# Performance work log

Hardware: AMD Instinct MI355X
Metric: run time of the kernel (lower is better)

The kernel has to match this reference:

```python
import jax, jax.numpy as jnp
import numpy as np

EPS = 1e-5

def _conv(x, w, pad, groups=1):
    return jax.lax.conv_general_dilated(
        x, w, window_strides=(1, 1), padding=[(pad, pad), (pad, pad)],
        dimension_numbers=('NCHW', 'OIHW', 'NCHW'), feature_group_count=groups)

def _bn(x, g, b, m, v):
    # inference batch-norm, per-channel
    s = g * jax.lax.rsqrt(v + EPS)
    return x * s[None, :, None, None] + (b - m * s)[None, :, None, None]

def setup_inputs() -> dict:
    key = jax.random.key(0)
    ks = jax.random.split(key, 20)
    B, C, H, W = 32, 128, 64, 64
    cs = C // 2  # c_split = 64
    d = {
        'x': jax.random.normal(ks[0], (B, C, H, W), jnp.float32),
        'weights': jax.random.uniform(ks[1], (B, 2), jnp.float32),
        'indices': jax.random.randint(ks[2], (B, 2), 0, 4, jnp.int32),
        # expert 0: Conv(cs -> C, k=3, p=1) + BN + SiLU
        'e0_w': jax.random.normal(ks[3], (C, cs, 3, 3), jnp.float32) * 0.05,
        'e0_g': jax.random.uniform(ks[4], (C,), jnp.float32, 0.5, 1.5),
        'e0_b': jax.random.normal(ks[5], (C,), jnp.float32) * 0.1,
        'e0_m': jax.random.normal(ks[6], (C,), jnp.float32) * 0.1,
        'e0_v': jax.random.uniform(ks[7], (C,), jnp.float32, 0.5, 1.5),
        # expert 1: depthwise 5x5 (cs, groups=cs) -> 1x1 (cs -> C) -> BN -> SiLU
        'e1_dw': jax.random.normal(ks[8], (cs, 1, 5, 5), jnp.float32) * 0.05,
        'e1_pw': jax.random.normal(ks[9], (C, cs, 1, 1), jnp.float32) * 0.05,
        'e1_g': jax.random.uniform(ks[10], (C,), jnp.float32, 0.5, 1.5),
        'e1_b': jax.random.normal(ks[11], (C,), jnp.float32) * 0.1,
        'e1_m': jax.random.normal(ks[12], (C,), jnp.float32) * 0.1,
        'e1_v': jax.random.uniform(ks[13], (C,), jnp.float32, 0.5, 1.5),
        # expert 2: GhostConv(C -> C): cv1 = Conv(C, C//2, 3), cv2 = Conv(C//2, C//2, 5, groups=C//2)
        'e2a_w': jax.random.normal(ks[14], (cs, C, 3, 3), jnp.float32) * 0.05,
        'e2a_g': jax.random.uniform(ks[15], (cs,), jnp.float32, 0.5, 1.5),
        'e2a_b': jax.random.normal(ks[16], (cs,), jnp.float32) * 0.1,
        'e2a_m': jax.random.normal(ks[17], (cs,), jnp.float32) * 0.1,
        'e2a_v': jax.random.uniform(ks[18], (cs,), jnp.float32, 0.5, 1.5),
        'e2b_w': jax.random.normal(ks[19], (cs, 1, 5, 5), jnp.float32) * 0.05,
    }
    ks2 = jax.random.split(jax.random.key(1), 4)
    d['e2b_g'] = jax.random.uniform(ks2[0], (cs,), jnp.float32, 0.5, 1.5)
    d['e2b_b'] = jax.random.normal(ks2[1], (cs,), jnp.float32) * 0.1
    d['e2b_m'] = jax.random.normal(ks2[2], (cs,), jnp.float32) * 0.1
    d['e2b_v'] = jax.random.uniform(ks2[3], (cs,), jnp.float32, 0.5, 1.5)
    return d

def _forward(x, weights, indices,
             e0_w, e0_g, e0_b, e0_m, e0_v,
             e1_dw, e1_pw, e1_g, e1_b, e1_m, e1_v,
             e2a_w, e2a_g, e2a_b, e2a_m, e2a_v,
             e2b_w, e2b_g, e2b_b, e2b_m, e2b_v):
    C = x.shape[1]
    cs = C // 2
    x_rgb, x_ir = x[:, :cs], x[:, cs:]
    # expert outputs computed densely over the whole batch, masked combine below
    e0 = jax.nn.silu(_bn(_conv(x_rgb, e0_w, pad=1), e0_g, e0_b, e0_m, e0_v))
    e1 = jax.nn.silu(_bn(_conv(_conv(x_ir, e1_dw, pad=2, groups=cs), e1_pw, pad=0),
                         e1_g, e1_b, e1_m, e1_v))
    g1 = jax.nn.silu(_bn(_conv(x, e2a_w, pad=1), e2a_g, e2a_b, e2a_m, e2a_v))
    g2 = jax.nn.silu(_bn(_conv(g1, e2b_w, pad=2, groups=cs), e2b_g, e2b_b, e2b_m, e2b_v))
    e2 = jnp.concatenate([g1, g2], axis=1)
    out = jnp.zeros_like(x)
    K = indices.shape[1]
    for k in range(K):  # small fixed top-k loop
        idx = indices[:, k][:, None, None, None]          # [B,1,1,1]
        w = weights[:, k][:, None, None, None]            # [B,1,1,1]
        out = out + jnp.where(idx == 0, e0 * w, 0.0)
        out = out + jnp.where(idx == 1, e1 * w, 0.0)
        out = out + jnp.where(idx == 2, e2 * w, 0.0)
        out = out + jnp.where(idx == 3, x * 0.1, 0.0)
    return out

def reference(x, weights, indices,
              e0_w, e0_g, e0_b, e0_m, e0_v,
              e1_dw, e1_pw, e1_g, e1_b, e1_m, e1_v,
              e2a_w, e2a_g, e2a_b, e2a_m, e2a_v,
              e2b_w, e2b_g, e2b_b, e2b_m, e2b_v):
    return _forward(x, weights, indices,
                    e0_w, e0_g, e0_b, e0_m, e0_v,
                    e1_dw, e1_pw, e1_g, e1_b, e1_m, e1_v,
                    e2a_w, e2a_g, e2a_b, e2a_m, e2a_v,
                    e2b_w, e2b_g, e2b_b, e2b_m, e2b_v)
```

## Files before the change

kernel.cpp:

```cpp
#include <hip/hip_runtime.h>

#define B_  32
#define C_  128
#define CS  64
#define H_  64
#define W_  64
#define HW  (H_*W_)

typedef __attribute__((ext_vector_type(8))) short bf16x8_t;
typedef __attribute__((ext_vector_type(4))) float f32x4_t;
typedef unsigned short u16;
typedef unsigned int   u32;

__device__ __forceinline__ float silu_f(float v) { return v / (1.f + __expf(-v)); }

__device__ __forceinline__ u16 f2bf(float f) {
    u32 u = __float_as_uint(f);
    u = (u + 0x7FFFu + ((u >> 16) & 1u)) >> 16;
    return (u16)u;
}
__device__ __forceinline__ float bf2f(u16 u) {
    return __uint_as_float(((u32)u) << 16);
}
__device__ __forceinline__ u32 cvtpk(float a, float b) {
    u32 r;
    asm("v_cvt_pk_bf16_f32 %0, %1, %2" : "=v"(r) : "v"(a), "v"(b));
    return r;
}

__device__ __forceinline__ void get_coeffs(const float* __restrict__ wts,
                                           const int* __restrict__ idxs, int b,
                                           float& c0, float& c1, float& c2, float& cid) {
    int   i0 = idxs[b*2+0], i1 = idxs[b*2+1];
    float w0 = wts[b*2+0],  w1 = wts[b*2+1];
    c0  = (i0==0?w0:0.f)   + (i1==0?w1:0.f);
    c1  = (i0==1?w0:0.f)   + (i1==1?w1:0.f);
    c2  = (i0==2?w0:0.f)   + (i1==2?w1:0.f);
    cid = (i0==3?0.1f:0.f) + (i1==3?0.1f:0.f);
}

__global__ __launch_bounds__(256) void k_prep(
    const float* __restrict__ e0w, const float* __restrict__ e2aw, const float* __restrict__ e1pw,
    u16* __restrict__ Wt0f, u16* __restrict__ Wt2f, u16* __restrict__ Wt1f)
{
    const int i0 = blockIdx.x*256 + threadIdx.x, stride = gridDim.x*256;
    for (int i = i0; i < 73728; i += stride) {
        int j = i&7, lane = (i>>3)&63, cog = (i>>9)&7, kc = (i>>12)&1, tap = i>>13;
        int co = cog*16 + (lane&15), ci = kc*32 + (lane>>4)*8 + j;
        Wt0f[i] = f2bf(e0w[(size_t)(co*64 + ci)*9 + tap]);
    }
    for (int i = i0; i < 73728; i += stride) {
        int j = i&7, lane = (i>>3)&63, cog = (i>>9)&3, kc = (i>>11)&3, tap = i>>13;
        int co = cog*16 + (lane&15), ci = kc*32 + (lane>>4)*8 + j;
        Wt2f[i] = f2bf(e2aw[(size_t)(co*128 + ci)*9 + tap]);
    }
    for (int i = i0; i < 8192; i += stride) {
        int j = i&7, lane = (i>>3)&63, cog = (i>>9)&7, kc = (i>>12)&1;
        int co = cog*16 + (lane&15), ci = kc*32 + (lane>>4)*8 + j;
        Wt1f[i] = f2bf(e1pw[(size_t)co*64 + ci]);
    }
}

__device__ __forceinline__ void stage_x(
    const float* __restrict__ xb,
    char* lin, int orow0, int t)
{
    f32x4_t V0[8], V1[8];
    #pragma unroll
    for (int k = 0; k < 8; ++k) {
        const int u = t + k*256;
        const int quad = u & 15, r = (u >> 4) & 3, cp = u >> 6;
        const int hh = orow0 - 1 + r;
        const int hcl = (hh < 0) ? 0 : ((hh > 63) ? 63 : hh);
        const float* p0 = xb + (size_t)(2*cp)*HW + hcl*64 + quad*4;
        asm volatile("global_load_dwordx4 %0, %1, off" : "=v"(V0[k]) : "v"(p0));
        asm volatile("global_load_dwordx4 %0, %1, off" : "=v"(V1[k]) : "v"(p0 + HW));
    }
    asm volatile("s_waitcnt vmcnt(0)" ::: "memory");
    __builtin_amdgcn_sched_barrier(0);
    #pragma unroll
    for (int k = 0; k < 8; ++k) {
        const int u = t + k*256;
        const int quad = u & 15, r = (u >> 4) & 3, cp = u >> 6;
        const int hh = orow0 - 1 + r;
        const bool ok = (hh >= 0 && hh < H_);
        #pragma unroll
        for (int j = 0; j < 4; ++j) {
            const int p = r*66 + quad*4 + j + 1;
            const u32 a = ((u32)p*128 + (u32)cp*4) ^ (((u32)(p & 7)) << 4);
            float f0 = ok ? V0[k][j] : 0.f;
            float f1 = ok ? V1[k][j] : 0.f;
            *(u32*)(lin + a) = cvtpk(f0, f1);
        }
    }
    {
        const int cp = t & 31, side = (t >> 5) & 1, r = t >> 6;
        const int p = r*66 + side*65;
        const u32 a = ((u32)p*128 + (u32)cp*4) ^ (((u32)(p & 7)) << 4);
        *(u32*)(lin + a) = 0u;
    }
}

template<int NCF, int NPF, int TK, int COUT>
__device__ __forceinline__ void conv_pass(
    const char* lin, const u16* __restrict__ wb, int koff,
    int rbase, int pxbase, int l15, int kg,
    f32x4_t (&acc)[NCF][NPF])
{
    bf16x8_t A0[NCF], A1[NCF], A2[NCF];

    auto issueA = [&](int i, bf16x8_t (&dst)[NCF]) {
        const int tap = i >> 1, kcl = i & 1;
        const u16* wt = wb + (size_t)((tap*TK + koff + kcl)*(COUT/16))*512;
        #pragma unroll
        for (int cf = 0; cf < NCF; ++cf)
            asm volatile("global_load_dwordx4 %0, %1, off"
                         : "=v"(dst[cf]) : "v"(wt + ((size_t)cf << 9)));
    };
    auto ldsB = [&](int i, int pf) -> bf16x8_t {
        const int tap = i >> 1, kcl = i & 1;
        const int dh = tap / 3, dwp = tap % 3;
        const int p = (rbase + dh)*66 + pxbase + pf*16 + l15 + dwp;
        u32 a = (u32)p*128 + (u32)kcl*64 + (u32)kg*16;
        a ^= ((u32)(p & 7)) << 4;
        return *(const bf16x8_t*)(lin + a);
    };

    issueA(0, A0);
    issueA(1, A1);
    #pragma unroll
    for (int i = 0; i < 18; ++i) {
        if (i + 2 < 18) {
            const int s = (i + 2) % 3;
            if (s == 0)      issueA(i + 2, A0);
            else if (s == 1) issueA(i + 2, A1);
            else             issueA(i + 2, A2);
        }
        if (i < 16)       asm volatile("s_waitcnt vmcnt(8)" ::: "memory");
        else if (i == 16) asm volatile("s_waitcnt vmcnt(4)" ::: "memory");
        else              asm volatile("s_waitcnt vmcnt(0)" ::: "memory");
        __builtin_amdgcn_sched_barrier(0);
        bf16x8_t* ac = (i % 3 == 0) ? A0 : ((i % 3 == 1) ? A1 : A2);
        #pragma unroll
        for (int pf = 0; pf < NPF; ++pf) {
            bf16x8_t bfr = ldsB(i, pf);
            #pragma unroll
            for (int cf = 0; cf < NCF; ++cf)
                acc[cf][pf] = __builtin_amdgcn_mfma_f32_16x16x32_bf16(ac[cf], bfr, acc[cf][pf], 0, 0, 0);
        }
    }
}

__global__ __launch_bounds__(256, 3) void k_conv(
    const float* __restrict__ x,
    const float* __restrict__ wts, const int* __restrict__ idxs,
    const u16* __restrict__ Wt0f, const u16* __restrict__ Wt2f,
    const float* __restrict__ e0g, const float* __restrict__ e0b,
    const float* __restrict__ e0m, const float* __restrict__ e0v,
    const float* __restrict__ e2ag, const float* __restrict__ e2ab,
    const float* __restrict__ e2am, const float* __restrict__ e2av,
    float* __restrict__ out, u16* __restrict__ g1)
{
    __shared__ char lin[33792];
    const int b = blockIdx.y, orow0 = blockIdx.x*2, t = threadIdx.x;
    float c0, c1, c2, cid;
    get_coeffs(wts, idxs, b, c0, c1, c2, cid);

    const int lane = t & 63, l15 = lane & 15, kg = lane >> 4, wv = t >> 6;
    const float* xb = x + (size_t)b*C_*HW;

    if (blockIdx.z == 0) {
        if (c0 == 0.f) {
            for (int i = t; i < 4096; i += 256) {
                int ch = i >> 5, q = i & 31;
                size_t o = ((size_t)(b*C_+ch))*HW + (size_t)orow0*64 + q*4;
                float4 ov;
                if (cid != 0.f) {
                    float4 xv = *(const float4*)(x + o);
                    ov.x = cid*xv.x; ov.y = cid*xv.y; ov.z = cid*xv.z; ov.w = cid*xv.w;
                } else { ov.x = ov.y = ov.z = ov.w = 0.f; }
                *(float4*)(out + o) = ov;
            }
            return;
        }
        stage_x(xb, lin, orow0, t);
        __syncthreads();

        const int cw = wv >> 1, rw = wv & 1;
        const int cobase = cw*64;
        f32x4_t acc[4][4];
        #pragma unroll
        for (int cf = 0; cf < 4; ++cf)
            #pragma unroll
            for (int pf = 0; pf < 4; ++pf)
                acc[cf][pf] = (f32x4_t){0.f, 0.f, 0.f, 0.f};

        const u16* wb = Wt0f + (size_t)(cobase >> 4)*512 + (size_t)lane*8;
        conv_pass<4, 4, 2, 128>(lin, wb, 0, rw, 0, l15, kg, acc);

        #pragma unroll
        for (int cf = 0; cf < 4; ++cf) {
            float sarr[4], tarr[4];
            #pragma unroll
            for (int r = 0; r < 4; ++r) {
                int co = cobase + cf*16 + kg*4 + r;
                float s = e0g[co] * rsqrtf(e0v[co] + 1e-5f);
                sarr[r] = s; tarr[r] = e0b[co] - e0m[co]*s;
            }
            #pragma unroll
            for (int pf = 0; pf < 4; ++pf) {
                size_t rowoff = (size_t)(orow0 + rw)*64 + pf*16 + l15;
                #pragma unroll
                for (int r = 0; r < 4; ++r) {
                    int co = cobase + cf*16 + kg*4 + r;
                    float v = silu_f(acc[cf][pf][r]*sarr[r] + tarr[r]);
                    size_t o = ((size_t)(b*C_+co))*HW + rowoff;
                    float idv = (cid != 0.f) ? cid*x[o] : 0.f;
                    out[o] = c0*v + idv;
                }
            }
        }
    } else {
        if (c2 == 0.f) return;

        const int rw = wv >> 1, pw = wv & 1;
        const int pxbase = pw*32;
        f32x4_t acc[4][2];
        #pragma unroll
        for (int cf = 0; cf < 4; ++cf)
            #pragma unroll
            for (int pf = 0; pf < 2; ++pf)
                acc[cf][pf] = (f32x4_t){0.f, 0.f, 0.f, 0.f};

        const u16* wb = Wt2f + (size_t)lane*8;

        stage_x(xb, lin, orow0, t);
        __syncthreads();
        conv_pass<4, 2, 4, 64>(lin, wb, 0, rw, pxbase, l15, kg, acc);
        __syncthreads();
        stage_x(xb + (size_t)CS*HW, lin, orow0, t);
        __syncthreads();
        conv_pass<4, 2, 4, 64>(lin, wb, 2, rw, pxbase, l15, kg, acc);

        #pragma unroll
        for (int cf = 0; cf < 4; ++cf) {
            float sarr[4], tarr[4];
            #pragma unroll
            for (int r = 0; r < 4; ++r) {
                int co = cf*16 + kg*4 + r;
                float s = e2ag[co] * rsqrtf(e2av[co] + 1e-5f);
                sarr[r] = s; tarr[r] = e2ab[co] - e2am[co]*s;
            }
            #pragma unroll
            for (int pf = 0; pf < 2; ++pf) {
                size_t rowoff = (size_t)(orow0 + rw)*64 + pxbase + pf*16 + l15;
                #pragma unroll
                for (int r = 0; r < 4; ++r) {
                    int co = cf*16 + kg*4 + r;
                    float v = silu_f(acc[cf][pf][r]*sarr[r] + tarr[r]);
                    g1[((size_t)(b*CS+co))*HW + rowoff] = f2bf(v);
                }
            }
        }
    }
}

__global__ __launch_bounds__(256) void k_tail(
    const float* __restrict__ x, const u16* __restrict__ g1,
    const float* __restrict__ wts, const int* __restrict__ idxs,
    const float* __restrict__ e1dw, const u16* __restrict__ Wt1f,
    const float* __restrict__ e1g, const float* __restrict__ e1b,
    const float* __restrict__ e1m, const float* __restrict__ e1v,
    const float* __restrict__ e2bw,
    const float* __restrict__ e2bg, const float* __restrict__ e2bb,
    const float* __restrict__ e2bm, const float* __restrict__ e2bv,
    float* __restrict__ out)
{
    const int b = blockIdx.y, band = blockIdx.x, t = threadIdx.x;
    const int orow0 = band*2;

    float c0, c1, c2, cid;
    get_coeffs(wts, idxs, b, c0, c1, c2, cid);
    if (c1 == 0.f && c2 == 0.f) return;

    __shared__ u16  lin[6*64*70];
    __shared__ u16  lout[128*72];
    __shared__ float wl[64*26];

    const int lane = t & 63, chl = lane & 15, cs = lane >> 4;
    const int wv = t >> 6, outrow = wv & 1, chhalf = wv >> 1;
    const int l15 = lane & 15, kg = lane >> 4;

    if (c1 != 0.f) {
        for (int i = t; i < 64*25; i += 256) wl[(i/25)*26 + (i%25)] = e1dw[i];
        for (int i = t; i < 6*64*16; i += 256) {
            int q = i & 15, ch = (i >> 4) & 63, r = i >> 10;
            int hh = orow0 - 2 + r;
            u32 w0 = 0u, w1 = 0u;
            if (hh >= 0 && hh < H_) {
                float4 v = *(const float4*)(x + ((size_t)(b*C_ + CS + ch))*HW + hh*64 + q*4);
                w0 = cvtpk(v.x, v.y); w1 = cvtpk(v.z, v.w);
            }
            u32* dst = (u32*)&lin[(r*64 + ch)*70 + 2 + q*4];
            dst[0] = w0; dst[1] = w1;
        }
        for (int i = t; i < 6*64; i += 256) {
            int ch = i & 63, r = i >> 6;
            *(u32*)&lin[(r*64 + ch)*70]      = 0u;
            u32* e = (u32*)&lin[(r*64 + ch)*70 + 66];
            e[0] = 0u; e[1] = 0u;
        }
        __syncthreads();

        #pragma unroll
        for (int chi = 0; chi < 2; ++chi) {
            const int ch = chhalf*32 + chl + chi*16;
            const float* wch = &wl[ch*26];
            float accp[16];
            #pragma unroll
            for (int p = 0; p < 16; ++p) accp[p] = 0.f;
            #pragma unroll
            for (int kh = 0; kh < 5; ++kh) {
                const u16* src = &lin[((outrow + kh)*64 + ch)*70 + cs*16];
                float rb[20];
                #pragma unroll
                for (int k = 0; k < 10; ++k) {
                    u32 u = *(const u32*)(src + 2*k);
                    rb[2*k]   = __uint_as_float(u << 16);
                    rb[2*k+1] = __uint_as_float(u & 0xFFFF0000u);
                }
                #pragma unroll
                for (int kw = 0; kw < 5; ++kw) {
                    float wvv = wch[kh*5 + kw];
                    #pragma unroll
                    for (int p = 0; p < 16; ++p) accp[p] += rb[p+kw]*wvv;
                }
            }
            const int px0 = outrow*64 + cs*16;
            #pragma unroll
            for (int p = 0; p < 16; ++p) lout[(px0+p)*72 + ch] = f2bf(accp[p]);
        }
        __syncthreads();

        const int cw = wv >> 1, pwv = wv & 1;
        f32x4_t acc[4][4];
        #pragma unroll
        for (int cf = 0; cf < 4; ++cf)
            #pragma unroll
            for (int pf = 0; pf < 4; ++pf)
                acc[cf][pf] = (f32x4_t){0.f, 0.f, 0.f, 0.f};

        #pragma unroll
        for (int kc = 0; kc < 2; ++kc) {
            const u16* wt = Wt1f + (((size_t)(kc*8 + cw*4)) << 9) + lane*8;
            bf16x8_t af[4];
            #pragma unroll
            for (int cf = 0; cf < 4; ++cf) af[cf] = *(const bf16x8_t*)(wt + (cf << 9));
            const int k0 = kc*32 + kg*8;
            #pragma unroll
            for (int pf = 0; pf < 4; ++pf) {
                bf16x8_t bfr = *(const bf16x8_t*)&lout[(pwv*64 + pf*16 + l15)*72 + k0];
                #pragma unroll
                for (int cf = 0; cf < 4; ++cf)
                    acc[cf][pf] = __builtin_amdgcn_mfma_f32_16x16x32_bf16(af[cf], bfr, acc[cf][pf], 0, 0, 0);
            }
        }

        #pragma unroll
        for (int cf = 0; cf < 4; ++cf) {
            float sarr[4], tarr[4];
            #pragma unroll
            for (int r = 0; r < 4; ++r) {
                int co = cw*64 + cf*16 + kg*4 + r;
                float s = e1g[co] * rsqrtf(e1v[co] + 1e-5f);
                sarr[r] = s; tarr[r] = e1b[co] - e1m[co]*s;
            }
            #pragma unroll
            for (int pf = 0; pf < 4; ++pf) {
                int px = pwv*64 + pf*16 + l15;
                size_t rowoff = (size_t)(orow0 + (px>>6))*64 + (px&63);
                #pragma unroll
                for (int r = 0; r < 4; ++r) {
                    int co = cw*64 + cf*16 + kg*4 + r;
                    float v = silu_f(acc[cf][pf][r]*sarr[r] + tarr[r]);
                    out[((size_t)(b*C_+co))*HW + rowoff] += c1*v;
                }
            }
        }
    }

    if (c2 != 0.f) {
        __syncthreads();

        for (int i = t; i < 64*25; i += 256) wl[(i/25)*26 + (i%25)] = e2bw[i];
        for (int i = t; i < 6*64*16; i += 256) {
            int q = i & 15, ch = (i >> 4) & 63, r = i >> 10;
            int hh = orow0 - 2 + r;
            u32 w0 = 0u, w1 = 0u;
            if (hh >= 0 && hh < H_) {
                const u32* src = (const u32*)(g1 + ((size_t)(b*CS+ch))*HW + hh*64 + q*4);
                w0 = src[0]; w1 = src[1];
            }
            u32* dst = (u32*)&lin[(r*64 + ch)*70 + 2 + q*4];
            dst[0] = w0; dst[1] = w1;
        }
        for (int i = t; i < 6*64; i += 256) {
            int ch = i & 63, r = i >> 6;
            *(u32*)&lin[(r*64 + ch)*70] = 0u;
            u32* e = (u32*)&lin[(r*64 + ch)*70 + 66];
            e[0] = 0u; e[1] = 0u;
        }
        __syncthreads();

        for (int i = t; i < 2*64*16; i += 256) {
            int q = i & 15, ch = (i >> 4) & 63, r = i >> 10;
            const u16* src = &lin[((r+2)*64 + ch)*70 + 2 + q*4];
            float* op = out + ((size_t)(b*C_+ch))*HW + (size_t)(orow0+r)*64 + q*4;
            float4 ov = *(float4*)op;
            ov.x += c2*bf2f(src[0]); ov.y += c2*bf2f(src[1]);
            ov.z += c2*bf2f(src[2]); ov.w += c2*bf2f(src[3]);
            *(float4*)op = ov;
        }

        #pragma unroll
        for (int chi = 0; chi < 2; ++chi) {
            const int ch = chhalf*32 + chl + chi*16;
            const float* wch = &wl[ch*26];
            float accp[16];
            #pragma unroll
            for (int p = 0; p < 16; ++p) accp[p] = 0.f;
            #pragma unroll
            for (int kh = 0; kh < 5; ++kh) {
                const u16* src = &lin[((outrow + kh)*64 + ch)*70 + cs*16];
                float rb[20];
                #pragma unroll
                for (int k = 0; k < 10; ++k) {
                    u32 u = *(const u32*)(src + 2*k);
                    rb[2*k]   = __uint_as_float(u << 16);
                    rb[2*k+1] = __uint_as_float(u & 0xFFFF0000u);
                }
                #pragma unroll
                for (int kw = 0; kw < 5; ++kw) {
                    float wvv = wch[kh*5 + kw];
                    #pragma unroll
                    for (int p = 0; p < 16; ++p) accp[p] += rb[p+kw]*wvv;
                }
            }
            float s = e2bg[ch] * rsqrtf(e2bv[ch] + 1e-5f);
            float tt = e2bb[ch] - e2bm[ch]*s;
            float* op = out + ((size_t)(b*C_ + CS + ch))*HW + (size_t)(orow0+outrow)*64 + cs*16;
            #pragma unroll
            for (int q = 0; q < 4; ++q) {
                float4 ov = *(float4*)(op + q*4);
                ov.x += c2*silu_f(accp[q*4+0]*s + tt);
                ov.y += c2*silu_f(accp[q*4+1]*s + tt);
                ov.z += c2*silu_f(accp[q*4+2]*s + tt);
                ov.w += c2*silu_f(accp[q*4+3]*s + tt);
                *(float4*)(op + q*4) = ov;
            }
        }
    }
}

extern "C" void kernel_launch(void* const* d_in, const int* in_sizes, int n_in,
                              void* d_out, int out_size, void* d_ws, size_t ws_size,
                              hipStream_t stream) {
    const float* x    = (const float*)d_in[0];
    const float* wts  = (const float*)d_in[1];
    const int*   idxs = (const int*)  d_in[2];
    const float* e0w  = (const float*)d_in[3];
    const float* e0g  = (const float*)d_in[4];
    const float* e0b  = (const float*)d_in[5];
    const float* e0m  = (const float*)d_in[6];
    const float* e0v  = (const float*)d_in[7];
    const float* e1dw = (const float*)d_in[8];
    const float* e1pw = (const float*)d_in[9];
    const float* e1g  = (const float*)d_in[10];
    const float* e1b  = (const float*)d_in[11];
    const float* e1m  = (const float*)d_in[12];
    const float* e1v  = (const float*)d_in[13];
    const float* e2aw = (const float*)d_in[14];
    const float* e2ag = (const float*)d_in[15];
    const float* e2ab = (const float*)d_in[16];
    const float* e2am = (const float*)d_in[17];
    const float* e2av = (const float*)d_in[18];
    const float* e2bw = (const float*)d_in[19];
    const float* e2bg = (const float*)d_in[20];
    const float* e2bb = (const float*)d_in[21];
    const float* e2bm = (const float*)d_in[22];
    const float* e2bv = (const float*)d_in[23];

    float* out = (float*)d_out;

    u16* g1   = (u16*)d_ws;
    u16* Wt0f = g1 + (size_t)8388608;
    u16* Wt2f = Wt0f + 73728;
    u16* Wt1f = Wt2f + 73728;

    k_prep<<<128, 256, 0, stream>>>(e0w, e2aw, e1pw, Wt0f, Wt2f, Wt1f);
    k_conv<<<dim3(32, B_, 2), 256, 0, stream>>>(
        x, wts, idxs, Wt0f, Wt2f,
        e0g, e0b, e0m, e0v, e2ag, e2ab, e2am, e2av, out, g1);
    k_tail<<<dim3(32, B_), 256, 0, stream>>>(
        x, g1, wts, idxs, e1dw, Wt1f, e1g, e1b, e1m, e1v,
        e2bw, e2bg, e2bb, e2bm, e2bv, out);
}
```

Before: 97.08 us.

## Compact active conv work into a worklist consumed by persistent atomic-fetching blocks

The prep kernel now builds a compacted list of active work items (expert-0 conv bands, GhostConv cv1 bands, identity/zero-fill bands) from the routing indices. k_conv becomes a persistent kernel of 1024 blocks that grab items through a global atomic counter, instead of launching a full 3D grid where inactive blocks exit early. Occupancy is raised via launch bounds 4 to fit more resident blocks. This is meant to remove wasted block launches and tail imbalance, at the cost of atomic contention, extra barriers per item and possible register pressure from the higher occupancy target.

```diff
diff --git a/kernel.cpp b/kernel.cpp
--- a/kernel.cpp
+++ b/kernel.cpp
@@ -41,7 +41,9 @@
 
 __global__ __launch_bounds__(256) void k_prep(
     const float* __restrict__ e0w, const float* __restrict__ e2aw, const float* __restrict__ e1pw,
-    u16* __restrict__ Wt0f, u16* __restrict__ Wt2f, u16* __restrict__ Wt1f)
+    const float* __restrict__ wts, const int* __restrict__ idxs,
+    u16* __restrict__ Wt0f, u16* __restrict__ Wt2f, u16* __restrict__ Wt1f,
+    u32* __restrict__ wl)
 {
     const int i0 = blockIdx.x*256 + threadIdx.x, stride = gridDim.x*256;
     for (int i = i0; i < 73728; i += stride) {
@@ -58,6 +60,33 @@
         int j = i&7, lane = (i>>3)&63, cog = (i>>9)&7, kc = (i>>12)&1;
         int co = cog*16 + (lane&15), ci = kc*32 + (lane>>4)*8 + j;
         Wt1f[i] = f2bf(e1pw[(size_t)co*64 + ci]);
+    }
+
+    if (blockIdx.x == 0) {
+        __shared__ u32 base[3][32];
+        if (threadIdx.x == 0) {
+            u32 n = 0;
+            for (int tp = 0; tp < 3; ++tp)
+                for (int bb = 0; bb < 32; ++bb) {
+                    float c0, c1, c2, cid;
+                    get_coeffs(wts, idxs, bb, c0, c1, c2, cid);
+                    bool act = (tp == 0) ? (c0 != 0.f) : (tp == 1) ? (c2 != 0.f) : (c0 == 0.f);
+                    base[tp][bb] = act ? n : 0xFFFFFFFFu;
+                    if (act) n += 32;
+                }
+            wl[0] = 0u;
+            wl[1] = n;
+        }
+        __syncthreads();
+        if (threadIdx.x < 32) {
+            for (int tp = 0; tp < 3; ++tp)
+                for (int bb = 0; bb < 32; ++bb) {
+                    u32 bs = base[tp][bb];
+                    if (bs != 0xFFFFFFFFu)
+                        wl[2 + bs + threadIdx.x] =
+                            ((u32)tp << 12) | ((u32)bb << 5) | (u32)threadIdx.x;
+                }
+        }
     }
 }
 
@@ -151,7 +180,7 @@
     }
 }
 
-__global__ __launch_bounds__(256, 3) void k_conv(
+__global__ __launch_bounds__(256, 4) void k_conv(
     const float* __restrict__ x,
     const float* __restrict__ wts, const int* __restrict__ idxs,
     const u16* __restrict__ Wt0f, const u16* __restrict__ Wt2f,
@@ -159,18 +188,28 @@
     const float* __restrict__ e0m, const float* __restrict__ e0v,
     const float* __restrict__ e2ag, const float* __restrict__ e2ab,
     const float* __restrict__ e2am, const float* __restrict__ e2av,
-    float* __restrict__ out, u16* __restrict__ g1)
+    float* __restrict__ out, u16* __restrict__ g1, u32* __restrict__ wl)
 {
     __shared__ char lin[33792];
-    const int b = blockIdx.y, orow0 = blockIdx.x*2, t = threadIdx.x;
-    float c0, c1, c2, cid;
-    get_coeffs(wts, idxs, b, c0, c1, c2, cid);
-
+    __shared__ u32 s_item;
+    const int t = threadIdx.x;
+    const u32 n_items = wl[1];
     const int lane = t & 63, l15 = lane & 15, kg = lane >> 4, wv = t >> 6;
-    const float* xb = x + (size_t)b*C_*HW;
-
-    if (blockIdx.z == 0) {
-        if (c0 == 0.f) {
+
+    for (;;) {
+        __syncthreads();
+        if (t == 0) s_item = atomicAdd(&wl[0], 1u);
+        __syncthreads();
+        const u32 ii = s_item;
+        if (ii >= n_items) return;
+        const u32 item = wl[2 + ii];
+        const int tp = item >> 12, b = (item >> 5) & 31, band = item & 31;
+        const int orow0 = band*2;
+        float c0, c1, c2, cid;
+        get_coeffs(wts, idxs, b, c0, c1, c2, cid);
+        const float* xb = x + (size_t)b*C_*HW;
+
+        if (tp == 2) {
             for (int i = t; i < 4096; i += 256) {
                 int ch = i >> 5, q = i & 31;
                 size_t o = ((size_t)(b*C_+ch))*HW + (size_t)orow0*64 + q*4;
@@ -181,84 +220,85 @@
                 } else { ov.x = ov.y = ov.z = ov.w = 0.f; }
                 *(float4*)(out + o) = ov;
             }
-            return;
-        }
-        stage_x(xb, lin, orow0, t);
-        __syncthreads();
-
-        const int cw = wv >> 1, rw = wv & 1;
-        const int cobase = cw*64;
-        f32x4_t acc[4][4];
-        #pragma unroll
-        for (int cf = 0; cf < 4; ++cf)
-            #pragma unroll
-            for (int pf = 0; pf < 4; ++pf)
-                acc[cf][pf] = (f32x4_t){0.f, 0.f, 0.f, 0.f};
-
-        const u16* wb = Wt0f + (size_t)(cobase >> 4)*512 + (size_t)lane*8;
-        conv_pass<4, 4, 2, 128>(lin, wb, 0, rw, 0, l15, kg, acc);
-
-        #pragma unroll
-        for (int cf = 0; cf < 4; ++cf) {
-            float sarr[4], tarr[4];
-            #pragma unroll
-            for (int r = 0; r < 4; ++r) {
-                int co = cobase + cf*16 + kg*4 + r;
-                float s = e0g[co] * rsqrtf(e0v[co] + 1e-5f);
-                sarr[r] = s; tarr[r] = e0b[co] - e0m[co]*s;
-            }
-            #pragma unroll
-            for (int pf = 0; pf < 4; ++pf) {
-                size_t rowoff = (size_t)(orow0 + rw)*64 + pf*16 + l15;
+            continue;
+        }
+
+        if (tp == 0) {
+            stage_x(xb, lin, orow0, t);
+            __syncthreads();
+
+            const int cw = wv >> 1, rw = wv & 1;
+            const int cobase = cw*64;
+            f32x4_t acc[4][4];
+            #pragma unroll
+            for (int cf = 0; cf < 4; ++cf)
+                #pragma unroll
+                for (int pf = 0; pf < 4; ++pf)
+                    acc[cf][pf] = (f32x4_t){0.f, 0.f, 0.f, 0.f};
+
+            const u16* wb = Wt0f + (size_t)(cobase >> 4)*512 + (size_t)lane*8;
+            conv_pass<4, 4, 2, 128>(lin, wb, 0, rw, 0, l15, kg, acc);
+
+            #pragma unroll
+            for (int cf = 0; cf < 4; ++cf) {
+                float sarr[4], tarr[4];
                 #pragma unroll
                 for (int r = 0; r < 4; ++r) {
                     int co = cobase + cf*16 + kg*4 + r;
-                    float v = silu_f(acc[cf][pf][r]*sarr[r] + tarr[r]);
-                    size_t o = ((size_t)(b*C_+co))*HW + rowoff;
-                    float idv = (cid != 0.f) ? cid*x[o] : 0.f;
-                    out[o] = c0*v + idv;
-                }
-            }
-        }
-    } else {
-        if (c2 == 0.f) return;
-
-        const int rw = wv >> 1, pw = wv & 1;
-        const int pxbase = pw*32;
-        f32x4_t acc[4][2];
-        #pragma unroll
-        for (int cf = 0; cf < 4; ++cf)
-            #pragma unroll
-            for (int pf = 0; pf < 2; ++pf)
-                acc[cf][pf] = (f32x4_t){0.f, 0.f, 0.f, 0.f};
-
-        const u16* wb = Wt2f + (size_t)lane*8;
-
-        stage_x(xb, lin, orow0, t);
-        __syncthreads();
-        conv_pass<4, 2, 4, 64>(lin, wb, 0, rw, pxbase, l15, kg, acc);
-        __syncthreads();
-        stage_x(xb + (size_t)CS*HW, lin, orow0, t);
-        __syncthreads();
-        conv_pass<4, 2, 4, 64>(lin, wb, 2, rw, pxbase, l15, kg, acc);
-
-        #pragma unroll
-        for (int cf = 0; cf < 4; ++cf) {
-            float sarr[4], tarr[4];
-            #pragma unroll
-            for (int r = 0; r < 4; ++r) {
-                int co = cf*16 + kg*4 + r;
-                float s = e2ag[co] * rsqrtf(e2av[co] + 1e-5f);
-                sarr[r] = s; tarr[r] = e2ab[co] - e2am[co]*s;
-            }
-            #pragma unroll
-            for (int pf = 0; pf < 2; ++pf) {
-                size_t rowoff = (size_t)(orow0 + rw)*64 + pxbase + pf*16 + l15;
+                    float s = e0g[co] * rsqrtf(e0v[co] + 1e-5f);
+                    sarr[r] = s; tarr[r] = e0b[co] - e0m[co]*s;
+                }
+                #pragma unroll
+                for (int pf = 0; pf < 4; ++pf) {
+                    size_t rowoff = (size_t)(orow0 + rw)*64 + pf*16 + l15;
+                    #pragma unroll
+                    for (int r = 0; r < 4; ++r) {
+                        int co = cobase + cf*16 + kg*4 + r;
+                        float v = silu_f(acc[cf][pf][r]*sarr[r] + tarr[r]);
+                        size_t o = ((size_t)(b*C_+co))*HW + rowoff;
+                        float idv = (cid != 0.f) ? cid*x[o] : 0.f;
+                        out[o] = c0*v + idv;
+                    }
+                }
+            }
+        } else {
+            const int rw = wv >> 1, pw = wv & 1;
+            const int pxbase = pw*32;
+            f32x4_t acc[4][2];
+            #pragma unroll
+            for (int cf = 0; cf < 4; ++cf)
+                #pragma unroll
+                for (int pf = 0; pf < 2; ++pf)
+                    acc[cf][pf] = (f32x4_t){0.f, 0.f, 0.f, 0.f};
+
+            const u16* wb = Wt2f + (size_t)lane*8;
+
+            stage_x(xb, lin, orow0, t);
+            __syncthreads();
+            conv_pass<4, 2, 4, 64>(lin, wb, 0, rw, pxbase, l15, kg, acc);
+            __syncthreads();
+            stage_x(xb + (size_t)CS*HW, lin, orow0, t);
+            __syncthreads();
+            conv_pass<4, 2, 4, 64>(lin, wb, 2, rw, pxbase, l15, kg, acc);
+
+            #pragma unroll
+            for (int cf = 0; cf < 4; ++cf) {
+                float sarr[4], tarr[4];
                 #pragma unroll
                 for (int r = 0; r < 4; ++r) {
                     int co = cf*16 + kg*4 + r;
-                    float v = silu_f(acc[cf][pf][r]*sarr[r] + tarr[r]);
-                    g1[((size_t)(b*CS+co))*HW + rowoff] = f2bf(v);
+                    float s = e2ag[co] * rsqrtf(e2av[co] + 1e-5f);
+                    sarr[r] = s; tarr[r] = e2ab[co] - e2am[co]*s;
+                }
+                #pragma unroll
+                for (int pf = 0; pf < 2; ++pf) {
+                    size_t rowoff = (size_t)(orow0 + rw)*64 + pxbase + pf*16 + l15;
+                    #pragma unroll
+                    for (int r = 0; r < 4; ++r) {
+                        int co = cf*16 + kg*4 + r;
+                        float v = silu_f(acc[cf][pf][r]*sarr[r] + tarr[r]);
+                        g1[((size_t)(b*CS+co))*HW + rowoff] = f2bf(v);
+                    }
                 }
             }
         }
@@ -496,11 +536,12 @@
     u16* Wt0f = g1 + (size_t)8388608;
     u16* Wt2f = Wt0f + 73728;
     u16* Wt1f = Wt2f + 73728;
-
-    k_prep<<<128, 256, 0, stream>>>(e0w, e2aw, e1pw, Wt0f, Wt2f, Wt1f);
-    k_conv<<<dim3(32, B_, 2), 256, 0, stream>>>(
+    u32* wl   = (u32*)(Wt1f + 8192);
+
+    k_prep<<<128, 256, 0, stream>>>(e0w, e2aw, e1pw, wts, idxs, Wt0f, Wt2f, Wt1f, wl);
+    k_conv<<<1024, 256, 0, stream>>>(
         x, wts, idxs, Wt0f, Wt2f,
-        e0g, e0b, e0m, e0v, e2ag, e2ab, e2am, e2av, out, g1);
+        e0g, e0b, e0m, e0v, e2ag, e2ab, e2am, e2av, out, g1, wl);
     k_tail<<<dim3(32, B_), 256, 0, stream>>>(
         x, g1, wts, idxs, e1dw, Wt1f, e1g, e1b, e1m, e1v,
         e2bw, e2bg, e2bb, e2bm, e2bv, out);
```

New measurement: 384.1 us. 3.96x slower.

## Fuse expert-1 depthwise+pointwise path into conv kernel, split e2b into own kernel

Applied to the files above, without the earlier changes.

Moves the expert-1 computation (depthwise 5x5 followed by the 1x1 MFMA pointwise conv) out of the tail kernel and into the z=0 blocks of k_conv. These blocks now write e0 plus identity and then accumulate e1 into out from the same block, using a unified 51 KB shared buffer with channels staged in two halves. The remaining e2b depthwise stage gets its own kernel. This removes a second full read-modify-write of the output for the e1 path and balances work across launches. The cost is higher LDS use in k_conv, which may lower occupancy under its launch bounds of 3 blocks per CU, and extra serialization inside the fused blocks.

```diff
diff --git a/kernel.cpp b/kernel.cpp
--- a/kernel.cpp
+++ b/kernel.cpp
@@ -159,9 +159,12 @@
     const float* __restrict__ e0m, const float* __restrict__ e0v,
     const float* __restrict__ e2ag, const float* __restrict__ e2ab,
     const float* __restrict__ e2am, const float* __restrict__ e2av,
+    const float* __restrict__ e1dw, const u16* __restrict__ Wt1f,
+    const float* __restrict__ e1g, const float* __restrict__ e1b,
+    const float* __restrict__ e1m, const float* __restrict__ e1v,
     float* __restrict__ out, u16* __restrict__ g1)
 {
-    __shared__ char lin[33792];
+    __shared__ char uni[51968];
     const int b = blockIdx.y, orow0 = blockIdx.x*2, t = threadIdx.x;
     float c0, c1, c2, cid;
     get_coeffs(wts, idxs, b, c0, c1, c2, cid);
@@ -169,25 +172,58 @@
     const int lane = t & 63, l15 = lane & 15, kg = lane >> 4, wv = t >> 6;
     const float* xb = x + (size_t)b*C_*HW;
 
-    if (blockIdx.z == 0) {
-        if (c0 == 0.f) {
-            for (int i = t; i < 4096; i += 256) {
-                int ch = i >> 5, q = i & 31;
-                size_t o = ((size_t)(b*C_+ch))*HW + (size_t)orow0*64 + q*4;
-                float4 ov;
-                if (cid != 0.f) {
-                    float4 xv = *(const float4*)(x + o);
-                    ov.x = cid*xv.x; ov.y = cid*xv.y; ov.z = cid*xv.z; ov.w = cid*xv.w;
-                } else { ov.x = ov.y = ov.z = ov.w = 0.f; }
-                *(float4*)(out + o) = ov;
-            }
-            return;
-        }
-        stage_x(xb, lin, orow0, t);
+    if (blockIdx.z == 1) {
+        if (c2 == 0.f) return;
+
+        const int rw = wv >> 1, pw = wv & 1;
+        const int pxbase = pw*32;
+        f32x4_t acc[4][2];
+        #pragma unroll
+        for (int cf = 0; cf < 4; ++cf)
+            #pragma unroll
+            for (int pf = 0; pf < 2; ++pf)
+                acc[cf][pf] = (f32x4_t){0.f, 0.f, 0.f, 0.f};
+
+        const u16* wb = Wt2f + (size_t)lane*8;
+
+        stage_x(xb, uni, orow0, t);
         __syncthreads();
-
-        const int cw = wv >> 1, rw = wv & 1;
-        const int cobase = cw*64;
+        conv_pass<4, 2, 4, 64>(uni, wb, 0, rw, pxbase, l15, kg, acc);
+        __syncthreads();
+        stage_x(xb + (size_t)CS*HW, uni, orow0, t);
+        __syncthreads();
+        conv_pass<4, 2, 4, 64>(uni, wb, 2, rw, pxbase, l15, kg, acc);
+
+        #pragma unroll
+        for (int cf = 0; cf < 4; ++cf) {
+            float sarr[4], tarr[4];
+            #pragma unroll
+            for (int r = 0; r < 4; ++r) {
+                int co = cf*16 + kg*4 + r;
+                float s = e2ag[co] * rsqrtf(e2av[co] + 1e-5f);
+                sarr[r] = s; tarr[r] = e2ab[co] - e2am[co]*s;
+            }
+            #pragma unroll
+            for (int pf = 0; pf < 2; ++pf) {
+                size_t rowoff = (size_t)(orow0 + rw)*64 + pxbase + pf*16 + l15;
+                #pragma unroll
+                for (int r = 0; r < 4; ++r) {
+                    int co = cf*16 + kg*4 + r;
+                    float v = silu_f(acc[cf][pf][r]*sarr[r] + tarr[r]);
+                    g1[((size_t)(b*CS+co))*HW + rowoff] = f2bf(v);
+                }
+            }
+        }
+        return;
+    }
+
+    const int cw = wv >> 1, rw = wv & 1;
+    const int cobase = cw*64;
+
+    if (c0 != 0.f) {
+        stage_x(xb, uni, orow0, t);
+        __syncthreads();
+
         f32x4_t acc[4][4];
         #pragma unroll
         for (int cf = 0; cf < 4; ++cf)
@@ -196,7 +232,7 @@
                 acc[cf][pf] = (f32x4_t){0.f, 0.f, 0.f, 0.f};
 
         const u16* wb = Wt0f + (size_t)(cobase >> 4)*512 + (size_t)lane*8;
-        conv_pass<4, 4, 2, 128>(lin, wb, 0, rw, 0, l15, kg, acc);
+        conv_pass<4, 4, 2, 128>(uni, wb, 0, rw, 0, l15, kg, acc);
 
         #pragma unroll
         for (int cf = 0; cf < 4; ++cf) {
@@ -220,108 +256,74 @@
                 }
             }
         }
+    } else if (c1 == 0.f) {
+        for (int i = t; i < 4096; i += 256) {
+            int ch = i >> 5, q = i & 31;
+            size_t o = ((size_t)(b*C_+ch))*HW + (size_t)orow0*64 + q*4;
+            float4 ov;
+            if (cid != 0.f) {
+                float4 xv = *(const float4*)(x + o);
+                ov.x = cid*xv.x; ov.y = cid*xv.y; ov.z = cid*xv.z; ov.w = cid*xv.w;
+            } else { ov.x = ov.y = ov.z = ov.w = 0.f; }
+            *(float4*)(out + o) = ov;
+        }
+        return;
     } else {
-        if (c2 == 0.f) return;
-
-        const int rw = wv >> 1, pw = wv & 1;
-        const int pxbase = pw*32;
-        f32x4_t acc[4][2];
         #pragma unroll
         for (int cf = 0; cf < 4; ++cf)
             #pragma unroll
-            for (int pf = 0; pf < 2; ++pf)
-                acc[cf][pf] = (f32x4_t){0.f, 0.f, 0.f, 0.f};
-
-        const u16* wb = Wt2f + (size_t)lane*8;
-
-        stage_x(xb, lin, orow0, t);
-        __syncthreads();
-        conv_pass<4, 2, 4, 64>(lin, wb, 0, rw, pxbase, l15, kg, acc);
-        __syncthreads();
-        stage_x(xb + (size_t)CS*HW, lin, orow0, t);
-        __syncthreads();
-        conv_pass<4, 2, 4, 64>(lin, wb, 2, rw, pxbase, l15, kg, acc);
-
-        #pragma unroll
-        for (int cf = 0; cf < 4; ++cf) {
-            float sarr[4], tarr[4];
-            #pragma unroll
-            for (int r = 0; r < 4; ++r) {
-                int co = cf*16 + kg*4 + r;
-                float s = e2ag[co] * rsqrtf(e2av[co] + 1e-5f);
-                sarr[r] = s; tarr[r] = e2ab[co] - e2am[co]*s;
-            }
-            #pragma unroll
-            for (int pf = 0; pf < 2; ++pf) {
-                size_t rowoff = (size_t)(orow0 + rw)*64 + pxbase + pf*16 + l15;
+            for (int pf = 0; pf < 4; ++pf) {
+                size_t rowoff = (size_t)(orow0 + rw)*64 + pf*16 + l15;
                 #pragma unroll
                 for (int r = 0; r < 4; ++r) {
-                    int co = cf*16 + kg*4 + r;
-                    float v = silu_f(acc[cf][pf][r]*sarr[r] + tarr[r]);
-                    g1[((size_t)(b*CS+co))*HW + rowoff] = f2bf(v);
+                    int co = cobase + cf*16 + kg*4 + r;
+                    size_t o = ((size_t)(b*C_+co))*HW + rowoff;
+                    out[o] = (cid != 0.f) ? cid*x[o] : 0.f;
                 }
             }
-        }
-    }
-}
-
-__global__ __launch_bounds__(256) void k_tail(
-    const float* __restrict__ x, const u16* __restrict__ g1,
-    const float* __restrict__ wts, const int* __restrict__ idxs,
-    const float* __restrict__ e1dw, const u16* __restrict__ Wt1f,
-    const float* __restrict__ e1g, const float* __restrict__ e1b,
-    const float* __restrict__ e1m, const float* __restrict__ e1v,
-    const float* __restrict__ e2bw,
-    const float* __restrict__ e2bg, const float* __restrict__ e2bb,
-    const float* __restrict__ e2bm, const float* __restrict__ e2bv,
-    float* __restrict__ out)
-{
-    const int b = blockIdx.y, band = blockIdx.x, t = threadIdx.x;
-    const int orow0 = band*2;
-
-    float c0, c1, c2, cid;
-    get_coeffs(wts, idxs, b, c0, c1, c2, cid);
-    if (c1 == 0.f && c2 == 0.f) return;
-
-    __shared__ u16  lin[6*64*70];
-    __shared__ u16  lout[128*72];
-    __shared__ float wl[64*26];
-
-    const int lane = t & 63, chl = lane & 15, cs = lane >> 4;
-    const int wv = t >> 6, outrow = wv & 1, chhalf = wv >> 1;
-    const int l15 = lane & 15, kg = lane >> 4;
-
-    if (c1 != 0.f) {
-        for (int i = t; i < 64*25; i += 256) wl[(i/25)*26 + (i%25)] = e1dw[i];
-        for (int i = t; i < 6*64*16; i += 256) {
-            int q = i & 15, ch = (i >> 4) & 63, r = i >> 10;
+    }
+
+    if (c1 == 0.f) return;
+
+    u16*   lin2 = (u16*)uni;
+    u16*   lout = (u16*)(uni + 26880);
+    float* wlf  = (float*)(uni + 45312);
+
+    __syncthreads();
+    for (int i = t; i < 64*25; i += 256) wlf[(i/25)*26 + (i%25)] = e1dw[i];
+
+    #pragma unroll
+    for (int pass = 0; pass < 2; ++pass) {
+        if (pass) __syncthreads();
+        for (int i = t; i < 6*32*16; i += 256) {
+            int q = i & 15, chs = (i >> 4) & 31, r = i >> 9;
             int hh = orow0 - 2 + r;
             u32 w0 = 0u, w1 = 0u;
             if (hh >= 0 && hh < H_) {
-                float4 v = *(const float4*)(x + ((size_t)(b*C_ + CS + ch))*HW + hh*64 + q*4);
+                float4 v = *(const float4*)(x + ((size_t)(b*C_ + CS + pass*32 + chs))*HW + hh*64 + q*4);
                 w0 = cvtpk(v.x, v.y); w1 = cvtpk(v.z, v.w);
             }
-            u32* dst = (u32*)&lin[(r*64 + ch)*70 + 2 + q*4];
+            u32* dst = (u32*)&lin2[(r*32 + chs)*70 + 2 + q*4];
             dst[0] = w0; dst[1] = w1;
         }
-        for (int i = t; i < 6*64; i += 256) {
-            int ch = i & 63, r = i >> 6;
-            *(u32*)&lin[(r*64 + ch)*70]      = 0u;
-            u32* e = (u32*)&lin[(r*64 + ch)*70 + 66];
+        for (int i = t; i < 6*32; i += 256) {
+            int chs = i & 31, r = i >> 5;
+            *(u32*)&lin2[(r*32 + chs)*70] = 0u;
+            u32* e = (u32*)&lin2[(r*32 + chs)*70 + 66];
             e[0] = 0u; e[1] = 0u;
         }
         __syncthreads();
 
-        #pragma unroll
-        for (int chi = 0; chi < 2; ++chi) {
-            const int ch = chhalf*32 + chl + chi*16;
-            const float* wch = &wl[ch*26];
+        {
+            const int outrow = wv & 1, cgrp = wv >> 1;
+            const int chloc = cgrp*16 + l15, cs_ = kg;
+            const float* wch = &wlf[(pass*32 + chloc)*26];
             float accp[16];
             #pragma unroll
             for (int p = 0; p < 16; ++p) accp[p] = 0.f;
             #pragma unroll
             for (int kh = 0; kh < 5; ++kh) {
-                const u16* src = &lin[((outrow + kh)*64 + ch)*70 + cs*16];
+                const u16* src = &lin2[((outrow + kh)*32 + chloc)*70 + cs_*16];
                 float rb[20];
                 #pragma unroll
                 for (int k = 0; k < 10; ++k) {
@@ -336,19 +338,22 @@
                     for (int p = 0; p < 16; ++p) accp[p] += rb[p+kw]*wvv;
                 }
             }
-            const int px0 = outrow*64 + cs*16;
-            #pragma unroll
-            for (int p = 0; p < 16; ++p) lout[(px0+p)*72 + ch] = f2bf(accp[p]);
-        }
-        __syncthreads();
-
-        const int cw = wv >> 1, pwv = wv & 1;
-        f32x4_t acc[4][4];
+            const int px0 = outrow*64 + cs_*16;
+            #pragma unroll
+            for (int p = 0; p < 16; ++p)
+                lout[(px0+p)*72 + pass*32 + chloc] = f2bf(accp[p]);
+        }
+    }
+    __syncthreads();
+
+    {
+        const int pwv = rw;
+        f32x4_t acc1[4][4];
         #pragma unroll
         for (int cf = 0; cf < 4; ++cf)
             #pragma unroll
             for (int pf = 0; pf < 4; ++pf)
-                acc[cf][pf] = (f32x4_t){0.f, 0.f, 0.f, 0.f};
+                acc1[cf][pf] = (f32x4_t){0.f, 0.f, 0.f, 0.f};
 
         #pragma unroll
         for (int kc = 0; kc < 2; ++kc) {
@@ -362,7 +367,7 @@
                 bf16x8_t bfr = *(const bf16x8_t*)&lout[(pwv*64 + pf*16 + l15)*72 + k0];
                 #pragma unroll
                 for (int cf = 0; cf < 4; ++cf)
-                    acc[cf][pf] = __builtin_amdgcn_mfma_f32_16x16x32_bf16(af[cf], bfr, acc[cf][pf], 0, 0, 0);
+                    acc1[cf][pf] = __builtin_amdgcn_mfma_f32_16x16x32_bf16(af[cf], bfr, acc1[cf][pf], 0, 0, 0);
             }
         }
 
@@ -377,87 +382,101 @@
             }
             #pragma unroll
             for (int pf = 0; pf < 4; ++pf) {
-                int px = pwv*64 + pf*16 + l15;
-                size_t rowoff = (size_t)(orow0 + (px>>6))*64 + (px&63);
+                size_t rowoff = (size_t)(orow0 + pwv)*64 + pf*16 + l15;
                 #pragma unroll
                 for (int r = 0; r < 4; ++r) {
                     int co = cw*64 + cf*16 + kg*4 + r;
-                    float v = silu_f(acc[cf][pf][r]*sarr[r] + tarr[r]);
+                    float v = silu_f(acc1[cf][pf][r]*sarr[r] + tarr[r]);
                     out[((size_t)(b*C_+co))*HW + rowoff] += c1*v;
                 }
             }
         }
     }
-
-    if (c2 != 0.f) {
-        __syncthreads();
-
-        for (int i = t; i < 64*25; i += 256) wl[(i/25)*26 + (i%25)] = e2bw[i];
-        for (int i = t; i < 6*64*16; i += 256) {
-            int q = i & 15, ch = (i >> 4) & 63, r = i >> 10;
-            int hh = orow0 - 2 + r;
-            u32 w0 = 0u, w1 = 0u;
-            if (hh >= 0 && hh < H_) {
-                const u32* src = (const u32*)(g1 + ((size_t)(b*CS+ch))*HW + hh*64 + q*4);
-                w0 = src[0]; w1 = src[1];
-            }
-            u32* dst = (u32*)&lin[(r*64 + ch)*70 + 2 + q*4];
-            dst[0] = w0; dst[1] = w1;
-        }
-        for (int i = t; i < 6*64; i += 256) {
-            int ch = i & 63, r = i >> 6;
-            *(u32*)&lin[(r*64 + ch)*70] = 0u;
-            u32* e = (u32*)&lin[(r*64 + ch)*70 + 66];
-            e[0] = 0u; e[1] = 0u;
-        }
-        __syncthreads();
-
-        for (int i = t; i < 2*64*16; i += 256) {
-            int q = i & 15, ch = (i >> 4) & 63, r = i >> 10;
-            const u16* src = &lin[((r+2)*64 + ch)*70 + 2 + q*4];
-            float* op = out + ((size_t)(b*C_+ch))*HW + (size_t)(orow0+r)*64 + q*4;
-            float4 ov = *(float4*)op;
-            ov.x += c2*bf2f(src[0]); ov.y += c2*bf2f(src[1]);
-            ov.z += c2*bf2f(src[2]); ov.w += c2*bf2f(src[3]);
-            *(float4*)op = ov;
-        }
-
-        #pragma unroll
-        for (int chi = 0; chi < 2; ++chi) {
-            const int ch = chhalf*32 + chl + chi*16;
-            const float* wch = &wl[ch*26];
-            float accp[16];
-            #pragma unroll
-            for (int p = 0; p < 16; ++p) accp[p] = 0.f;
-            #pragma unroll
-            for (int kh = 0; kh < 5; ++kh) {
-                const u16* src = &lin[((outrow + kh)*64 + ch)*70 + cs*16];
-                float rb[20];
-                #pragma unroll
-                for (int k = 0; k < 10; ++k) {
-                    u32 u = *(const u32*)(src + 2*k);
-                    rb[2*k]   = __uint_as_float(u << 16);
-                    rb[2*k+1] = __uint_as_float(u & 0xFFFF0000u);
-                }
-                #pragma unroll
-                for (int kw = 0; kw < 5; ++kw) {
-                    float wvv = wch[kh*5 + kw];
-                    #pragma unroll
-                    for (int p = 0; p < 16; ++p) accp[p] += rb[p+kw]*wvv;
-                }
-            }
-            float s = e2bg[ch] * rsqrtf(e2bv[ch] + 1e-5f);
-            float tt = e2bb[ch] - e2bm[ch]*s;
-            float* op = out + ((size_t)(b*C_ + CS + ch))*HW + (size_t)(orow0+outrow)*64 + cs*16;
-            #pragma unroll
-            for (int q = 0; q < 4; ++q) {
-                float4 ov = *(float4*)(op + q*4);
-                ov.x += c2*silu_f(accp[q*4+0]*s + tt);
-                ov.y += c2*silu_f(accp[q*4+1]*s + tt);
-                ov.z += c2*silu_f(accp[q*4+2]*s + tt);
-                ov.w += c2*silu_f(accp[q*4+3]*s + tt);
-                *(float4*)(op + q*4) = ov;
-            }
+}
+
+__global__ __launch_bounds__(256) void k_e2b(
+    const u16* __restrict__ g1, const float* __restrict__ wts, const int* __restrict__ idxs,
+    const float* __restrict__ dww, const float* __restrict__ gg, const float* __restrict__ bb,
+    const float* __restrict__ mm, const float* __restrict__ vv, float* __restrict__ out)
+{
+    const int b = blockIdx.y, band = blockIdx.x, t = threadIdx.x;
+    const int orow0 = band*2;
+
+    float c0, c1, c2, cid;
+    get_coeffs(wts, idxs, b, c0, c1, c2, cid);
+    if (c2 == 0.f) return;
+
+    __shared__ u16  lin[6*64*70];
+    __shared__ float wl[64*26];
+
+    for (int i = t; i < 64*25; i += 256) wl[(i/25)*26 + (i%25)] = dww[i];
+    for (int i = t; i < 6*64*16; i += 256) {
+        int q = i & 15, ch = (i >> 4) & 63, r = i >> 10;
+        int hh = orow0 - 2 + r;
+        u32 w0 = 0u, w1 = 0u;
+        if (hh >= 0 && hh < H_) {
+            const u32* src = (const u32*)(g1 + ((size_t)(b*CS+ch))*HW + hh*64 + q*4);
+            w0 = src[0]; w1 = src[1];
+        }
+        u32* dst = (u32*)&lin[(r*64 + ch)*70 + 2 + q*4];
+        dst[0] = w0; dst[1] = w1;
+    }
+    for (int i = t; i < 6*64; i += 256) {
+        int ch = i & 63, r = i >> 6;
+        *(u32*)&lin[(r*64 + ch)*70] = 0u;
+        u32* e = (u32*)&lin[(r*64 + ch)*70 + 66];
+        e[0] = 0u; e[1] = 0u;
+    }
+    __syncthreads();
+
+    for (int i = t; i < 2*64*16; i += 256) {
+        int q = i & 15, ch = (i >> 4) & 63, r = i >> 10;
+        const u16* src = &lin[((r+2)*64 + ch)*70 + 2 + q*4];
+        float* op = out + ((size_t)(b*C_+ch))*HW + (size_t)(orow0+r)*64 + q*4;
+        float4 ov = *(float4*)op;
+        ov.x += c2*bf2f(src[0]); ov.y += c2*bf2f(src[1]);
+        ov.z += c2*bf2f(src[2]); ov.w += c2*bf2f(src[3]);
+        *(float4*)op = ov;
+    }
+
+    const int lane = t & 63, chl = lane & 15, cs = lane >> 4;
+    const int wv = t >> 6, outrow = wv & 1, chhalf = wv >> 1;
+
+    #pragma unroll
+    for (int chi = 0; chi < 2; ++chi) {
+        const int ch = chhalf*32 + chl + chi*16;
+        const float* wch = &wl[ch*26];
+        float accp[16];
+        #pragma unroll
+        for (int p = 0; p < 16; ++p) accp[p] = 0.f;
+        #pragma unroll
+        for (int kh = 0; kh < 5; ++kh) {
+            const u16* src = &lin[((outrow + kh)*64 + ch)*70 + cs*16];
+            float rb[20];
+            #pragma unroll
+            for (int k = 0; k < 10; ++k) {
+                u32 u = *(const u32*)(src + 2*k);
+                rb[2*k]   = __uint_as_float(u << 16);
+                rb[2*k+1] = __uint_as_float(u & 0xFFFF0000u);
+            }
+            #pragma unroll
+            for (int kw = 0; kw < 5; ++kw) {
+                float wvv = wch[kh*5 + kw];
+                #pragma unroll
+                for (int p = 0; p < 16; ++p) accp[p] += rb[p+kw]*wvv;
+            }
+        }
+        float s = gg[ch] * rsqrtf(vv[ch] + 1e-5f);
+        float tt = bb[ch] - mm[ch]*s;
+        float* op = out + ((size_t)(b*C_ + CS + ch))*HW + (size_t)(orow0+outrow)*64 + cs*16;
+        #pragma unroll
+        for (int q = 0; q < 4; ++q) {
+            float4 ov = *(float4*)(op + q*4);
+            ov.x += c2*silu_f(accp[q*4+0]*s + tt);
+            ov.y += c2*silu_f(accp[q*4+1]*s + tt);
+            ov.z += c2*silu_f(accp[q*4+2]*s + tt);
+            ov.w += c2*silu_f(accp[q*4+3]*s + tt);
+            *(float4*)(op + q*4) = ov;
         }
     }
 }
@@ -500,8 +519,8 @@
     k_prep<<<128, 256, 0, stream>>>(e0w, e2aw, e1pw, Wt0f, Wt2f, Wt1f);
     k_conv<<<dim3(32, B_, 2), 256, 0, stream>>>(
         x, wts, idxs, Wt0f, Wt2f,
-        e0g, e0b, e0m, e0v, e2ag, e2ab, e2am, e2av, out, g1);
-    k_tail<<<dim3(32, B_), 256, 0, stream>>>(
-        x, g1, wts, idxs, e1dw, Wt1f, e1g, e1b, e1m, e1v,
-        e2bw, e2bg, e2bb, e2bm, e2bv, out);
-}
+        e0g, e0b, e0m, e0v, e2ag, e2ab, e2am, e2av,
+        e1dw, Wt1f, e1g, e1b, e1m, e1v, out, g1);
+    k_e2b<<<dim3(32, B_), 256, 0, stream>>>(
+        g1, wts, idxs, e2bw, e2bg, e2bb, e2bm, e2bv, out);
+}
```

New measurement: 93.01 us (median of 3 runs). -4.2%, faster.
